# Optimization experiments

Hardware: AMD Instinct MI355X
Metric: run time of the kernel (lower is better)

## Reference

```python
import jax, jax.numpy as jnp
import numpy as np

N = 65536   # query points
M = 65536   # support points
H = 32      # neighbors per query
IN = 64     # input feature dim
OUT = 64    # out_dim // 2
K = 15      # kernel points
EXTENT = 0.1 * 1.2 / 2.5  # radius * kp_extent / conv_radius = 0.048
BN_EPS = 1e-5


def setup_inputs() -> dict:
    key = jax.random.key(0)
    ks = jax.random.split(key, 8)
    x = jax.random.normal(ks[0], (M, IN), dtype=jnp.float32)
    q_pts = jax.random.uniform(ks[1], (N, 3), dtype=jnp.float32) * 0.1
    s_pts = jax.random.uniform(ks[2], (M, 3), dtype=jnp.float32) * 0.1
    neighb_inds = jax.random.randint(ks[3], (N, H), 0, M, dtype=jnp.int32)
    kernel_points = jax.random.normal(ks[4], (K, 3), dtype=jnp.float32) * (0.5 * EXTENT)
    weights = jax.random.normal(ks[5], (K, IN, OUT), dtype=jnp.float32) * 0.05
    gamma = jnp.ones((OUT,), dtype=jnp.float32)
    beta = jnp.zeros((OUT,), dtype=jnp.float32)
    return {"x": x, "q_pts": q_pts, "s_pts": s_pts, "neighb_inds": neighb_inds,
            "kernel_points": kernel_points, "weights": weights,
            "gamma": gamma, "beta": beta}


def reference(x, q_pts, s_pts, neighb_inds, kernel_points, weights, gamma, beta):
    # --- KPConv (rigid, linear influence, sum aggregation) ---
    # Shadow point/feature for out-of-range neighbor indices (KPConv convention).
    s_pad = jnp.concatenate([s_pts, jnp.full((1, 3), 1e6, s_pts.dtype)], axis=0)
    x_pad = jnp.concatenate([x, jnp.zeros((1, x.shape[1]), x.dtype)], axis=0)

    # Relative neighbor coordinates: [N, H, 3]
    neighbors = s_pad[neighb_inds] - q_pts[:, None, :]
    # Squared distance to each kernel point: [N, H, K]
    diffs = neighbors[:, :, None, :] - kernel_points[None, None, :, :]
    sq_dist = jnp.sum(diffs * diffs, axis=-1)
    # Linear kernel-point influence, clipped at 0: [N, H, K]
    all_weights = jnp.maximum(1.0 - jnp.sqrt(sq_dist) / EXTENT, 0.0)

    # Gather neighbor features: [N, H, IN]
    neighb_x = x_pad[neighb_inds]
    # Influence-weighted aggregation per kernel point: [N, K, IN]
    weighted = jnp.einsum('nhk,nhi->nki', all_weights, neighb_x)
    # Apply per-kernel-point weight matrices and sum over kernel points: [N, OUT]
    out = jnp.einsum('nki,kio->no', weighted, weights)

    # --- BatchNorm (training-mode statistics over points) ---
    mean = jnp.mean(out, axis=0)
    var = jnp.var(out, axis=0)
    out = (out - mean) / jnp.sqrt(var + BN_EPS) * gamma + beta

    # --- LeakyReLU(0.1) ---
    return jnp.where(out >= 0, out, 0.1 * out)
```

## Files before the change

kernel.cpp:

```cpp
#include <hip/hip_runtime.h>
#include <math.h>

#define NQ   65536
#define H    32
#define IN   64
#define OUTC 64
#define K    15
#define QB   16
#define S_XN 68
#define S_WT 36
#define AK   72
#define AROW 1076
#define INV_EXT (1.0f / 0.048f)

#define OFF_PSUM  131072
#define OFF_SCSH  (OFF_PSUM + 2097152)
#define OFF_XBF   (OFF_SCSH + 1024)
#define NEED_BF16 (OFF_XBF + (size_t)NQ * IN * 2)

typedef __attribute__((ext_vector_type(8))) short short8;
typedef __attribute__((ext_vector_type(4))) short short4v;
typedef __attribute__((ext_vector_type(4))) float float4v;

static __device__ __forceinline__ unsigned short f2bf(float f) {
    return (unsigned short)((__float_as_uint(f) + 0x8000u) >> 16);
}
static __device__ __forceinline__ unsigned pk2(float a, float b) {
    return (__float_as_uint(a) + 0x8000u) >> 16 |
           ((__float_as_uint(b) + 0x8000u) & 0xFFFF0000u);
}

__global__ __launch_bounds__(256) void prep_all(
    const float* __restrict__ W, const float* __restrict__ x,
    short* __restrict__ Bfrag, unsigned short* __restrict__ xbf, int do_x)
{
    const int b = blockIdx.x;
    if (b < 4096) {
        if (do_x) {
            const int t = b * 256 + threadIdx.x;
            const float4 v = ((const float4*)x)[t];
            uint2 p; p.x = pk2(v.x, v.y); p.y = pk2(v.z, v.w);
            ((uint2*)xbf)[t] = p;
        }
    } else {
        const int t2 = (b - 4096) * 256 + threadIdx.x;
        const int o  = t2 & 63;
        const int i  = (t2 >> 6) & 63;
        const int kq = t2 >> 12;
        const int t  = kq * 2 + (i >> 5);
        const int lane = ((i >> 3) & 3) * 16 + (o & 15);
        const int v  = o >> 4;
        const int j  = i & 7;
        Bfrag[((v * 30 + t) * 64 + lane) * 8 + j] = (short)f2bf(W[t2]);
    }
}

template<bool BFX>
__global__ __launch_bounds__(256, 4) void kpconv_mfma(
    const float* __restrict__ x, const unsigned short* __restrict__ xbf,
    const float* __restrict__ qp, const float* __restrict__ sp,
    const int* __restrict__ inds, const float* __restrict__ kp,
    const short* __restrict__ Bfrag, float* __restrict__ out_raw,
    float* __restrict__ psum)
{
    __shared__ __align__(16) short lds[17920];
    short* xn  = lds;
    short* wT  = lds + 8704;
    short* Awt = lds;

    const int tid  = threadIdx.x;
    const int lane = tid & 63;
    const int wv   = tid >> 6;
    const int quad = lane >> 4;
    const int ml   = lane & 15;
    const int q0   = blockIdx.x * QB;

    short* xn_own = xn + wv * (H * S_XN);

    short4v xv[4][8];
    float4  xf[4][8];
#pragma unroll
    for (int qi = 0; qi < 4; ++qi) {
        const int ibase = (q0 + wv * 4 + qi) * H;
#pragma unroll
        for (int j = 0; j < 8; ++j) {
            const int id = inds[ibase + j * 4 + quad];
            if (BFX) xv[qi][j] = *(const short4v*)((const short*)xbf + id * IN + ml * 4);
            else     xf[qi][j] = *(const float4*)(x + id * IN + ml * 4);
        }
    }

    for (int rep = 0; rep < 2; ++rep) {
        const int p = lane + rep * 64;
        const int qi = p >> 5, h = p & 31;
        const int qg = wv * 4 + qi;
        const int n = q0 + qg;
        const int id = inds[n * H + h];
        const float dx = sp[id * 3 + 0] - qp[n * 3 + 0];
        const float dy = sp[id * 3 + 1] - qp[n * 3 + 1];
        const float dz = sp[id * 3 + 2] - qp[n * 3 + 2];
#pragma unroll
        for (int k = 0; k < K; ++k) {
            const float ex = dx - kp[k * 3 + 0];
            const float ey = dy - kp[k * 3 + 1];
            const float ez = dz - kp[k * 3 + 2];
            const float sq = ex * ex + ey * ey + ez * ez;
            float wval = 1.0f - __builtin_amdgcn_sqrtf(sq) * INV_EXT;
            wval = wval > 0.0f ? wval : 0.0f;
            wT[(qg * 16 + k) * S_WT + h] = (short)f2bf(wval);
        }
        wT[(qg * 16 + K) * S_WT + h] = 0;
    }

    float4v frag[4][4];
#pragma unroll
    for (int qi = 0; qi < 4; ++qi)
#pragma unroll
        for (int v = 0; v < 4; ++v) frag[qi][v] = (float4v){0.f, 0.f, 0.f, 0.f};

#pragma unroll
    for (int qi = 0; qi < 4; ++qi) {
        const int qg = wv * 4 + qi;

#pragma unroll
        for (int j = 0; j < 8; ++j) {
            const int h = j * 4 + quad;
            if (BFX) {
                *(short4v*)&xn_own[h * S_XN + ml * 4] = xv[qi][j];
            } else {
                short4v p;
                p[0] = (short)f2bf(xf[qi][j].x); p[1] = (short)f2bf(xf[qi][j].y);
                p[2] = (short)f2bf(xf[qi][j].z); p[3] = (short)f2bf(xf[qi][j].w);
                *(short4v*)&xn_own[h * S_XN + ml * 4] = p;
            }
        }

        const int arow = (qg * 16 + ml) * S_WT + quad * 8;
        const short4v alo = *(const short4v*)&wT[arow];
        const short4v ahi = *(const short4v*)&wT[arow + 4];
        short8 a;
#pragma unroll
        for (int e = 0; e < 4; ++e) { a[e] = alo[e]; a[e + 4] = ahi[e]; }

#pragma unroll
        for (int v = 0; v < 4; ++v) {
            short8 bb;
#pragma unroll
            for (int j = 0; j < 8; ++j)
                bb[j] = xn_own[(quad * 8 + j) * S_XN + v * 16 + ml];
            frag[qi][v] = __builtin_amdgcn_mfma_f32_16x16x32_bf16(a, bb, frag[qi][v], 0, 0, 0);
        }
    }

    __syncthreads();

#pragma unroll
    for (int qi = 0; qi < 4; ++qi) {
        const int qg = wv * 4 + qi;
#pragma unroll
        for (int v = 0; v < 4; ++v) {
#pragma unroll
            for (int r = 0; r < 4; ++r) {
                const int kq = quad * 4 + r;
                if (kq < K)
                    Awt[qg * AROW + kq * AK + v * 16 + ml] = (short)f2bf(frag[qi][v][r]);
            }
        }
    }
    __syncthreads();

    float4v acc = (float4v){0.f, 0.f, 0.f, 0.f};
    const short* bptr = Bfrag + (wv * 30) * 512 + lane * 8;
#pragma unroll 2
    for (int t = 0; t < 30; ++t) {
        const int abase = ml * AROW + (t >> 1) * AK + (t & 1) * 32 + quad * 8;
        const short4v alo = *(const short4v*)&Awt[abase];
        const short4v ahi = *(const short4v*)&Awt[abase + 4];
        short8 a;
#pragma unroll
        for (int e = 0; e < 4; ++e) { a[e] = alo[e]; a[e + 4] = ahi[e]; }
        const short8 bb = *(const short8*)(bptr + t * 512);
        acc = __builtin_amdgcn_mfma_f32_16x16x32_bf16(a, bb, acc, 0, 0, 0);
    }

    float s = 0.f, s2 = 0.f;
#pragma unroll
    for (int r = 0; r < 4; ++r) {
        const float v = acc[r];
        out_raw[(q0 + quad * 4 + r) * OUTC + wv * 16 + ml] = v;
        s += v; s2 += v * v;
    }
    s  += __shfl_xor(s, 16, 64);  s  += __shfl_xor(s, 32, 64);
    s2 += __shfl_xor(s2, 16, 64); s2 += __shfl_xor(s2, 32, 64);
    if (quad == 0) {
        const int c = wv * 16 + ml;
        psum[c * 4096 + blockIdx.x]          = s;
        psum[262144 + c * 4096 + blockIdx.x] = s2;
    }
}

__global__ __launch_bounds__(256) void bn_stats(
    const float* __restrict__ psum, const float* __restrict__ gamma,
    const float* __restrict__ beta, float* __restrict__ sc_sh)
{
    const int c = blockIdx.x;
    const int t = threadIdx.x;
    float s = 0.f, q = 0.f;
#pragma unroll
    for (int i = 0; i < 16; ++i) {
        s += psum[c * 4096 + t + i * 256];
        q += psum[262144 + c * 4096 + t + i * 256];
    }
    __shared__ float rs[4], rq[4];
#pragma unroll
    for (int off = 32; off; off >>= 1) {
        s += __shfl_down(s, off, 64);
        q += __shfl_down(q, off, 64);
    }
    if ((t & 63) == 0) { rs[t >> 6] = s; rq[t >> 6] = q; }
    __syncthreads();
    if (t == 0) {
        s = rs[0] + rs[1] + rs[2] + rs[3];
        q = rq[0] + rq[1] + rq[2] + rq[3];
        const float mean = s * (1.0f / (float)NQ);
        const float var  = q * (1.0f / (float)NQ) - mean * mean;
        const float scale = gamma[c] / sqrtf(var + 1e-5f);
        sc_sh[c]      = scale;
        sc_sh[64 + c] = beta[c] - mean * scale;
    }
}

__global__ __launch_bounds__(256) void bn_apply(
    float* __restrict__ out, const float* __restrict__ sc_sh)
{
    __shared__ float sc[64];
    __shared__ float sh[64];
    if (threadIdx.x < 64) {
        sc[threadIdx.x] = sc_sh[threadIdx.x];
        sh[threadIdx.x] = sc_sh[64 + threadIdx.x];
    }
    __syncthreads();
    const int idx = blockIdx.x * 256 + threadIdx.x;
#pragma unroll
    for (int it = 0; it < 4; ++it) {
        const int e = idx + it * 262144;
        float4 v = ((const float4*)out)[e];
        const int cg = (e & 15) * 4;
        float4 r;
        r.x = v.x * sc[cg + 0] + sh[cg + 0];
        r.y = v.y * sc[cg + 1] + sh[cg + 1];
        r.z = v.z * sc[cg + 2] + sh[cg + 2];
        r.w = v.w * sc[cg + 3] + sh[cg + 3];
        r.x = r.x >= 0.0f ? r.x : 0.1f * r.x;
        r.y = r.y >= 0.0f ? r.y : 0.1f * r.y;
        r.z = r.z >= 0.0f ? r.z : 0.1f * r.z;
        r.w = r.w >= 0.0f ? r.w : 0.1f * r.w;
        ((float4*)out)[e] = r;
    }
}

extern "C" void kernel_launch(void* const* d_in, const int* in_sizes, int n_in,
                              void* d_out, int out_size, void* d_ws, size_t ws_size,
                              hipStream_t stream)
{
    (void)in_sizes; (void)n_in; (void)out_size;
    const float* x     = (const float*)d_in[0];
    const float* qp    = (const float*)d_in[1];
    const float* sp    = (const float*)d_in[2];
    const int*   inds  = (const int*)d_in[3];
    const float* kp    = (const float*)d_in[4];
    const float* W     = (const float*)d_in[5];
    const float* gamma = (const float*)d_in[6];
    const float* beta  = (const float*)d_in[7];
    float* out = (float*)d_out;

    short*          Bfrag = (short*)d_ws;
    float*          psum  = (float*)((char*)d_ws + OFF_PSUM);
    float*          sc_sh = (float*)((char*)d_ws + OFF_SCSH);
    unsigned short* xbf   = (unsigned short*)((char*)d_ws + OFF_XBF);

    const int use_bf = (ws_size >= NEED_BF16) ? 1 : 0;

    prep_all<<<4336, 256, 0, stream>>>(W, x, Bfrag, xbf, use_bf);
    if (use_bf)
        kpconv_mfma<true><<<NQ / QB, 256, 0, stream>>>(x, xbf, qp, sp, inds, kp, Bfrag, out, psum);
    else
        kpconv_mfma<false><<<NQ / QB, 256, 0, stream>>>(x, xbf, qp, sp, inds, kp, Bfrag, out, psum);
    bn_stats<<<64, 256, 0, stream>>>(psum, gamma, beta, sc_sh);
    bn_apply<<<1024, 256, 0, stream>>>(out, sc_sh);
}
```

Before: 150.0 us.

## Use transposing LDS reads and XOR-swizzled layouts in KPConv MFMA kernel

Reorganizes the LDS layouts for neighbor features and kernel-point influence weights so the first MFMA stage can load operands with ds_read_b64_tr_b16 transposing reads instead of scalar strided 16-bit loads. The intermediate weighted-feature tile is stored with an XOR swizzle in a kernel-point-major layout padded to 16, and the pre-packed weight fragments are regenerated to match (32 k-steps including zero padding). LDS shrinks and launch bounds rise to 5 blocks per CU for more occupancy. This targets LDS bank conflicts and per-element load instruction counts, at the cost of two extra zero-padded MFMA steps and inline asm with manual waitcnt.

```diff
diff --git a/kernel.cpp b/kernel.cpp
--- a/kernel.cpp
+++ b/kernel.cpp
@@ -7,10 +7,6 @@
 #define OUTC 64
 #define K    15
 #define QB   16
-#define S_XN 68
-#define S_WT 36
-#define AK   72
-#define AROW 1076
 #define INV_EXT (1.0f / 0.048f)
 
 #define OFF_PSUM  131072
@@ -43,62 +39,71 @@
             ((uint2*)xbf)[t] = p;
         }
     } else {
-        const int t2 = (b - 4096) * 256 + threadIdx.x;
-        const int o  = t2 & 63;
-        const int i  = (t2 >> 6) & 63;
-        const int kq = t2 >> 12;
-        const int t  = kq * 2 + (i >> 5);
-        const int lane = ((i >> 3) & 3) * 16 + (o & 15);
-        const int v  = o >> 4;
-        const int j  = i & 7;
-        Bfrag[((v * 30 + t) * 64 + lane) * 8 + j] = (short)f2bf(W[t2]);
+        const int t2  = (b - 4096) * 256 + threadIdx.x;
+        const int j   = t2 & 7;
+        const int ln  = (t2 >> 3) & 63;
+        const int tt  = (t2 >> 9) & 31;
+        const int wvq = t2 >> 14;
+        const int kp2 = tt * 32 + (ln >> 4) * 8 + j;
+        const int kq  = kp2 & 15;
+        const int ii  = kp2 >> 4;
+        const int oo  = wvq * 16 + (ln & 15);
+        const float val = (kq < K) ? W[(kq * 64 + ii) * 64 + oo] : 0.0f;
+        Bfrag[t2] = (short)f2bf(val);
     }
 }
 
 template<bool BFX>
-__global__ __launch_bounds__(256, 4) void kpconv_mfma(
+__global__ __launch_bounds__(256, 5) void kpconv_mfma(
     const float* __restrict__ x, const unsigned short* __restrict__ xbf,
     const float* __restrict__ qp, const float* __restrict__ sp,
     const int* __restrict__ inds, const float* __restrict__ kp,
     const short* __restrict__ Bfrag, float* __restrict__ out_raw,
     float* __restrict__ psum)
 {
-    __shared__ __align__(16) short lds[17920];
+    __shared__ __align__(16) short lds[16384];
     short* xn  = lds;
-    short* wT  = lds + 8704;
-    short* Awt = lds;
+    short* wT2 = lds + 8192;
 
     const int tid  = threadIdx.x;
     const int lane = tid & 63;
     const int wv   = tid >> 6;
     const int quad = lane >> 4;
     const int ml   = lane & 15;
+    const int q8   = lane >> 3;
+    const int m8   = lane & 7;
     const int q0   = blockIdx.x * QB;
 
-    short* xn_own = xn + wv * (H * S_XN);
-
-    short4v xv[4][8];
-    float4  xf[4][8];
+    short* xn_own = xn + wv * 2048;
+
+    short8 xv[4][4];
+    float4 xf[4][4][2];
 #pragma unroll
     for (int qi = 0; qi < 4; ++qi) {
         const int ibase = (q0 + wv * 4 + qi) * H;
 #pragma unroll
-        for (int j = 0; j < 8; ++j) {
-            const int id = inds[ibase + j * 4 + quad];
-            if (BFX) xv[qi][j] = *(const short4v*)((const short*)xbf + id * IN + ml * 4);
-            else     xf[qi][j] = *(const float4*)(x + id * IN + ml * 4);
-        }
-    }
-
+        for (int j = 0; j < 4; ++j) {
+            const int id = inds[ibase + j * 8 + q8];
+            if (BFX) {
+                xv[qi][j] = *(const short8*)((const short*)xbf + id * IN + m8 * 8);
+            } else {
+                xf[qi][j][0] = *(const float4*)(x + id * IN + m8 * 8);
+                xf[qi][j][1] = *(const float4*)(x + id * IN + m8 * 8 + 4);
+            }
+        }
+    }
+
+#pragma unroll
     for (int rep = 0; rep < 2; ++rep) {
-        const int p = lane + rep * 64;
+        const int p  = lane + rep * 64;
         const int qi = p >> 5, h = p & 31;
         const int qg = wv * 4 + qi;
-        const int n = q0 + qg;
+        const int n  = q0 + qg;
         const int id = inds[n * H + h];
         const float dx = sp[id * 3 + 0] - qp[n * 3 + 0];
         const float dy = sp[id * 3 + 1] - qp[n * 3 + 1];
         const float dz = sp[id * 3 + 2] - qp[n * 3 + 2];
+        short8 w0, w1;
 #pragma unroll
         for (int k = 0; k < K; ++k) {
             const float ex = dx - kp[k * 3 + 0];
@@ -107,10 +112,18 @@
             const float sq = ex * ex + ey * ey + ez * ez;
             float wval = 1.0f - __builtin_amdgcn_sqrtf(sq) * INV_EXT;
             wval = wval > 0.0f ? wval : 0.0f;
-            wT[(qg * 16 + k) * S_WT + h] = (short)f2bf(wval);
-        }
-        wT[(qg * 16 + K) * S_WT + h] = 0;
-    }
+            if (k < 8) w0[k]     = (short)f2bf(wval);
+            else       w1[k - 8] = (short)f2bf(wval);
+        }
+        w1[7] = 0;
+        short* dst = wT2 + qg * 512 + ((h >> 2) & 1) * 256 + (h >> 3) * 64 + (h & 3) * 16;
+        *(short8*)dst       = w0;
+        *(short8*)(dst + 8) = w1;
+    }
+
+    const unsigned ldsb = (unsigned)(size_t)(&lds[0]);
+    const unsigned xnb  = ldsb + (unsigned)(wv * 4096 + lane * 8);
+    const unsigned wtb  = ldsb + 16384u + (unsigned)(wv * 4096 + lane * 8);
 
     float4v frag[4][4];
 #pragma unroll
@@ -118,64 +131,80 @@
 #pragma unroll
         for (int v = 0; v < 4; ++v) frag[qi][v] = (float4v){0.f, 0.f, 0.f, 0.f};
 
+    const int Eb = (m8 >> 1) * 512 + ((q8 >> 2) & 1) * 256 + (q8 & 3) * 16 + (m8 & 1) * 8;
+
+#pragma unroll
+    for (int qi = 0; qi < 4; ++qi) {
+#pragma unroll
+        for (int j = 0; j < 4; ++j) {
+            short8 pv;
+            if (BFX) {
+                pv = xv[qi][j];
+            } else {
+                const float4 a0 = xf[qi][j][0], a1 = xf[qi][j][1];
+                pv[0] = (short)f2bf(a0.x); pv[1] = (short)f2bf(a0.y);
+                pv[2] = (short)f2bf(a0.z); pv[3] = (short)f2bf(a0.w);
+                pv[4] = (short)f2bf(a1.x); pv[5] = (short)f2bf(a1.y);
+                pv[6] = (short)f2bf(a1.z); pv[7] = (short)f2bf(a1.w);
+            }
+            *(short8*)&xn_own[Eb + j * 64] = pv;
+        }
+        __builtin_amdgcn_sched_barrier(0);
+
+        short4v a0, a1, b0[4], b1[4];
+        asm volatile("ds_read_b64_tr_b16 %0, %1 offset:%c2"
+                     : "=v"(a0) : "v"(wtb), "i"(qi * 1024) : "memory");
+        asm volatile("ds_read_b64_tr_b16 %0, %1 offset:%c2"
+                     : "=v"(a1) : "v"(wtb), "i"(qi * 1024 + 512) : "memory");
+#pragma unroll
+        for (int v = 0; v < 4; ++v) {
+            asm volatile("ds_read_b64_tr_b16 %0, %1 offset:%c2"
+                         : "=v"(b0[v]) : "v"(xnb), "i"(v * 1024) : "memory");
+            asm volatile("ds_read_b64_tr_b16 %0, %1 offset:%c2"
+                         : "=v"(b1[v]) : "v"(xnb), "i"(v * 1024 + 512) : "memory");
+        }
+        asm volatile("s_waitcnt lgkmcnt(0)");
+        __builtin_amdgcn_sched_barrier(0);
+
+        short8 a;
+#pragma unroll
+        for (int e = 0; e < 4; ++e) { a[e] = a0[e]; a[e + 4] = a1[e]; }
+#pragma unroll
+        for (int v = 0; v < 4; ++v) {
+            short8 bb;
+#pragma unroll
+            for (int e = 0; e < 4; ++e) { bb[e] = b0[v][e]; bb[e + 4] = b1[v][e]; }
+            frag[qi][v] = __builtin_amdgcn_mfma_f32_16x16x32_bf16(a, bb, frag[qi][v], 0, 0, 0);
+        }
+    }
+
+    __syncthreads();
+
+    char* AwtB = (char*)lds;
 #pragma unroll
     for (int qi = 0; qi < 4; ++qi) {
         const int qg = wv * 4 + qi;
-
-#pragma unroll
-        for (int j = 0; j < 8; ++j) {
-            const int h = j * 4 + quad;
-            if (BFX) {
-                *(short4v*)&xn_own[h * S_XN + ml * 4] = xv[qi][j];
-            } else {
-                short4v p;
-                p[0] = (short)f2bf(xf[qi][j].x); p[1] = (short)f2bf(xf[qi][j].y);
-                p[2] = (short)f2bf(xf[qi][j].z); p[3] = (short)f2bf(xf[qi][j].w);
-                *(short4v*)&xn_own[h * S_XN + ml * 4] = p;
-            }
-        }
-
-        const int arow = (qg * 16 + ml) * S_WT + quad * 8;
-        const short4v alo = *(const short4v*)&wT[arow];
-        const short4v ahi = *(const short4v*)&wT[arow + 4];
-        short8 a;
-#pragma unroll
-        for (int e = 0; e < 4; ++e) { a[e] = alo[e]; a[e + 4] = ahi[e]; }
-
+        char* qb = AwtB + qg * 2048;
+        const int xr = (qg & 7) << 4;
 #pragma unroll
         for (int v = 0; v < 4; ++v) {
-            short8 bb;
-#pragma unroll
-            for (int j = 0; j < 8; ++j)
-                bb[j] = xn_own[(quad * 8 + j) * S_XN + v * 16 + ml];
-            frag[qi][v] = __builtin_amdgcn_mfma_f32_16x16x32_bf16(a, bb, frag[qi][v], 0, 0, 0);
-        }
-    }
-
+            short4v w;
+#pragma unroll
+            for (int r = 0; r < 4; ++r) w[r] = (short)f2bf(frag[qi][v][r]);
+            *(short4v*)(qb + ((((v * 16 + ml) * 32) + quad * 8) ^ xr)) = w;
+        }
+    }
     __syncthreads();
 
-#pragma unroll
-    for (int qi = 0; qi < 4; ++qi) {
-        const int qg = wv * 4 + qi;
-#pragma unroll
-        for (int v = 0; v < 4; ++v) {
-#pragma unroll
-            for (int r = 0; r < 4; ++r) {
-                const int kq = quad * 4 + r;
-                if (kq < K)
-                    Awt[qg * AROW + kq * AK + v * 16 + ml] = (short)f2bf(frag[qi][v][r]);
-            }
-        }
-    }
-    __syncthreads();
-
     float4v acc = (float4v){0.f, 0.f, 0.f, 0.f};
-    const short* bptr = Bfrag + (wv * 30) * 512 + lane * 8;
+    const short* bptr = Bfrag + (wv * 32) * 512 + lane * 8;
+    const char*  arow = AwtB + ml * 2048;
+    const int    xr2  = (ml & 7) << 4;
 #pragma unroll 2
-    for (int t = 0; t < 30; ++t) {
-        const int abase = ml * AROW + (t >> 1) * AK + (t & 1) * 32 + quad * 8;
-        const short4v alo = *(const short4v*)&Awt[abase];
-        const short4v ahi = *(const short4v*)&Awt[abase + 4];
+    for (int t = 0; t < 32; ++t) {
+        const int byt = (t * 64 + quad * 16) ^ xr2;
+        const short4v alo = *(const short4v*)(arow + byt);
+        const short4v ahi = *(const short4v*)(arow + byt + 8);
         short8 a;
 #pragma unroll
         for (int e = 0; e < 4; ++e) { a[e] = alo[e]; a[e + 4] = ahi[e]; }
@@ -281,7 +310,7 @@
 
     const int use_bf = (ws_size >= NEED_BF16) ? 1 : 0;
 
-    prep_all<<<4336, 256, 0, stream>>>(W, x, Bfrag, xbf, use_bf);
+    prep_all<<<4352, 256, 0, stream>>>(W, x, Bfrag, xbf, use_bf);
     if (use_bf)
         kpconv_mfma<true><<<NQ / QB, 256, 0, stream>>>(x, xbf, qp, sp, inds, kp, Bfrag, out, psum);
     else
```

Result: no change. 150.2 us (+0.2%).
